# Kernel optimization log

Measured on AMD Instinct MI355X. Metric: run time of the kernel, lower is better.

## Reference

```python
import jax, jax.numpy as jnp
import numpy as np

STATE_LEN = 8
LAYER_NUM = 1
LN_EPS = 1e-5


def setup_inputs() -> dict:
    key = jax.random.key(0)
    ks = jax.random.split(key, 12)
    B, T, D = 4, 4096, 1024   # T = seq_len (4080) + 2*state_len (8)
    dk, dv = 128, 128
    s = 0.02
    f32 = jnp.float32
    return {
        "x": jax.random.normal(ks[0], (B, T, D), f32),
        # torch Linear(dim_input, 2*dim) without bias, stored as (in, out)
        "Wq": jax.random.normal(ks[1], (D, 2 * dk), f32) * s,
        "Wk": jax.random.normal(ks[2], (D, 2 * dk), f32) * s,
        "Wv": jax.random.normal(ks[3], (D, 2 * dv), f32) * s,
        "Wq_state": jax.random.normal(ks[4], (D, 2 * dk), f32) * s,
        "Wk_state": jax.random.normal(ks[5], (D, 2 * dk), f32) * s,
        "Wv_state": jax.random.normal(ks[6], (D, 2 * dv), f32) * s,
        "lambda_q1": jax.random.normal(ks[7], (1, dk), f32),
        "lambda_q2": jax.random.normal(ks[8], (1, dk), f32),
        "lambda_k1": jax.random.normal(ks[9], (dk, 1), f32),
        "lambda_k2": jax.random.normal(ks[10], (dk, 1), f32),
        "ln_gamma": jnp.ones((2 * dv,), f32),
        "ln_beta": jnp.zeros((2 * dv,), f32),
    }


def reference(x, Wq, Wk, Wv, Wq_state, Wk_state, Wv_state,
              lambda_q1, lambda_q2, lambda_k1, lambda_k2, ln_gamma, ln_beta):
    S = STATE_LEN
    lambda_init = 0.8 - 0.6 * np.exp(-0.3 * LAYER_NUM)  # python float, fp32-safe

    # extract_state: start state / middle / end state
    xs0, xm, xs1 = x[:, :S], x[:, S:-S], x[:, -S:]

    def proj(W, Ws):  # state tokens use *_state projections
        return jnp.concatenate([xs0 @ Ws, xm @ W, xs1 @ Ws], axis=1)

    q = proj(Wq, Wq_state)   # [B, T, 2*dk]
    k = proj(Wk, Wk_state)
    v = proj(Wv, Wv_state)   # [B, T, 2*dv]

    dk = Wq.shape[1] // 2
    q1, q2 = q[..., :dk], q[..., dk:]
    k1, k2 = k[..., :dk], k[..., dk:]

    T = q.shape[1]
    scale = 1.0 / jnp.sqrt(jnp.asarray(dk, q.dtype))  # SDPA default: 1/sqrt(dim_key)
    causal = jnp.tril(jnp.ones((T, T), dtype=bool))   # triu(-inf, diag=1) mask

    def attn(qh, kh):
        scores = jnp.einsum('btd,bsd->bts', qh, kh) * scale
        scores = jnp.where(causal, scores, -jnp.inf)
        p = jax.nn.softmax(scores, axis=-1)
        return jnp.einsum('bts,bse->bte', p, v)  # full 2*dv value

    att1 = attn(q1, k1)
    att2 = attn(q2, k2)

    lam = (jnp.exp(lambda_q1 @ lambda_k1) - jnp.exp(lambda_q2 @ lambda_k2))[0, 0] + lambda_init
    att = att1 - lam * att2  # [B, T, 2*dv]

    # out_norm: LayerNorm(2*dim_value, eps=1e-5)
    mu = jnp.mean(att, axis=-1, keepdims=True)
    var = jnp.var(att, axis=-1, keepdims=True)
    return (att - mu) / jnp.sqrt(var + LN_EPS) * ln_gamma + ln_beta
```

## Files before the change

### kernel.cpp

```cpp
#include <hip/hip_runtime.h>
#include <hip/hip_bf16.h>


typedef __bf16 bf16_t;
typedef __bf16 bf16x8 __attribute__((ext_vector_type(8)));
typedef __bf16 bf16x4 __attribute__((ext_vector_type(4)));
typedef float  f32x4  __attribute__((ext_vector_type(4)));

#define MFMA16(a, b, c) __builtin_amdgcn_mfma_f32_16x16x32_bf16((a), (b), (c), 0, 0, 0)

typedef __attribute__((address_space(1))) void glb_void;
typedef __attribute__((address_space(3))) void lds_void;

__device__ __forceinline__ void gld_lds16(void* dst, const void* src) {
  __builtin_amdgcn_global_load_lds((glb_void*)src, (lds_void*)dst, 16, 0, 0);
}

#define TSEQ 4096
#define C1f 0.12751744416f
#define C2f 4.3280851227f
#define LAM_INIT 0.3555090675909693f

__global__ void cvt_x_kernel(const float* __restrict__ x, bf16_t* __restrict__ xb) {
  size_t i = ((size_t)blockIdx.x * 256 + threadIdx.x) * 8;
  float4 a = *(const float4*)(x + i);
  float4 b = *(const float4*)(x + i + 4);
  bf16x8 o;
  o[0] = (bf16_t)a.x; o[1] = (bf16_t)a.y; o[2] = (bf16_t)a.z; o[3] = (bf16_t)a.w;
  o[4] = (bf16_t)b.x; o[5] = (bf16_t)b.y; o[6] = (bf16_t)b.z; o[7] = (bf16_t)b.w;
  *(bf16x8*)(xb + i) = o;
}

__global__ void cvt_w_kernel(const float* __restrict__ w0, const float* __restrict__ w1,
                             const float* __restrict__ w2, const float* __restrict__ w3,
                             const float* __restrict__ w4, const float* __restrict__ w5,
                             bf16_t* __restrict__ wt) {
  __shared__ float lt[64][68];
  const int mat = blockIdx.y;
  const int kt = blockIdx.x & 15, nt = blockIdx.x >> 4;
  const float* W = w0;
  if (mat == 1) W = w1; else if (mat == 2) W = w2; else if (mat == 3) W = w3;
  else if (mat == 4) W = w4; else if (mat == 5) W = w5;
  const int k0 = kt * 64, n0 = nt * 64;
  const int tid = threadIdx.x;
#pragma unroll
  for (int rnd = 0; rnd < 4; ++rnd) {
    int row = rnd * 16 + (tid >> 4);
    int c4 = (tid & 15) * 4;
    float4 v = *(const float4*)(W + (size_t)(k0 + row) * 256 + n0 + c4);
    *(float4*)&lt[row][c4] = v;
  }
  __syncthreads();
  const int n = tid >> 2;
  const int c16 = (tid & 3) * 16;
  bf16x8 o1, o2;
#pragma unroll
  for (int j = 0; j < 8; ++j) o1[j] = (bf16_t)lt[c16 + j][n];
#pragma unroll
  for (int j = 0; j < 8; ++j) o2[j] = (bf16_t)lt[c16 + 8 + j][n];
  bf16_t* dst = wt + (size_t)mat * 262144 + (size_t)(n0 + n) * 1024 + k0 + c16;
  *(bf16x8*)dst = o1;
  *(bf16x8*)(dst + 8) = o2;
}

__global__ void lam_kernel(const float* __restrict__ lq1, const float* __restrict__ lq2,
                           const float* __restrict__ lk1, const float* __restrict__ lk2,
                           float* __restrict__ lamout) {
  const int t = threadIdx.x;
  float s1 = lq1[2 * t] * lk1[2 * t] + lq1[2 * t + 1] * lk1[2 * t + 1];
  float s2 = lq2[2 * t] * lk2[2 * t] + lq2[2 * t + 1] * lk2[2 * t + 1];
#pragma unroll
  for (int m = 1; m < 64; m <<= 1) { s1 += __shfl_xor(s1, m); s2 += __shfl_xor(s2, m); }
  if (t == 0) *lamout = expf(s1) - expf(s2) + LAM_INIT;
}

__global__ __launch_bounds__(256, 2)
void proj_kernel(const bf16_t* __restrict__ xb, const bf16_t* __restrict__ wt,
                 bf16_t* __restrict__ qg, bf16_t* __restrict__ kg, bf16_t* __restrict__ vtg) {
  __shared__ __align__(16) char smem[49152];
  const int tid = threadIdx.x;
  const int w = tid >> 6;
  const int lane = tid & 63;
  const int l15 = lane & 15;
  const int g = lane >> 4;
  const int Mt = blockIdx.x;
  const int mat = blockIdx.y;
  const bf16_t* wmat = wt + (size_t)mat * 262144;
  const int row0 = Mt * 128;

  const f32x4 FZ = {0.f, 0.f, 0.f, 0.f};
  f32x4 acc[4][8];
#pragma unroll
  for (int i = 0; i < 4; ++i)
#pragma unroll
    for (int j = 0; j < 8; ++j) acc[i][j] = FZ;

  char* As = smem;
  char* Bs = smem + 16384;
  const int swz = (l15 & 7) << 4;

  for (int kt = 0; kt < 16; ++kt) {
    const int k0 = kt * 64;
#pragma unroll
    for (int rnd = 0; rnd < 4; ++rnd) {
      int arow = rnd * 32 + w * 8 + (lane >> 3);
      int m8 = lane & 7;
      const bf16_t* src = xb + (size_t)(row0 + arow) * 1024 + k0 + ((m8 ^ (arow & 7)) << 3);
      gld_lds16(As + rnd * 4096 + w * 1024, src);
    }
#pragma unroll
    for (int rnd = 0; rnd < 8; ++rnd) {
      int brow = rnd * 32 + w * 8 + (lane >> 3);
      int m8 = lane & 7;
      const bf16_t* src = wmat + (size_t)brow * 1024 + k0 + ((m8 ^ (brow & 7)) << 3);
      gld_lds16(Bs + rnd * 4096 + w * 1024, src);
    }
    __syncthreads();
    const int ab = (w >> 1) * 64;
    const int bb = (w & 1) * 128;
#pragma unroll
    for (int ks = 0; ks < 2; ++ks) {
      bf16x8 af[4], bfr[8];
#pragma unroll
      for (int mf = 0; mf < 4; ++mf) {
        int r = ab + mf * 16 + l15;
        af[mf] = *(const bf16x8*)(As + r * 128 + ((ks * 64 + g * 16) ^ swz));
      }
#pragma unroll
      for (int nf = 0; nf < 8; ++nf) {
        int c = bb + nf * 16 + l15;
        bfr[nf] = *(const bf16x8*)(Bs + c * 128 + ((ks * 64 + g * 16) ^ swz));
      }
#pragma unroll
      for (int mf = 0; mf < 4; ++mf)
#pragma unroll
        for (int nf = 0; nf < 8; ++nf)
          acc[mf][nf] = MFMA16(af[mf], bfr[nf], acc[mf][nf]);
    }
    __syncthreads();
  }

  const int ab = (w >> 1) * 64;
  const int bb = (w & 1) * 128;
  if (mat < 2) {
    bf16_t* og = (mat == 0) ? qg : kg;
#pragma unroll
    for (int mf = 0; mf < 4; ++mf)
#pragma unroll
      for (int nf = 0; nf < 8; ++nf) {
        int col = bb + nf * 16 + l15;
#pragma unroll
        for (int r = 0; r < 4; ++r) {
          int row = row0 + ab + mf * 16 + g * 4 + r;
          og[(size_t)row * 256 + col] = (bf16_t)acc[mf][nf][r];
        }
      }
  } else {
#pragma unroll
    for (int mf = 0; mf < 4; ++mf) {
      int t0 = row0 + ab + mf * 16 + g * 4;
      int bidx = t0 >> 12;
      int tt = t0 & 4095;
#pragma unroll
      for (int nf = 0; nf < 8; ++nf) {
        int col = bb + nf * 16 + l15;
        bf16x4 pk;
#pragma unroll
        for (int r = 0; r < 4; ++r) pk[r] = (bf16_t)acc[mf][nf][r];
        *(bf16x4*)(vtg + ((size_t)(bidx * 256 + col)) * 4096 + tt) = pk;
      }
    }
  }
}

__global__ void fixup_kernel(const bf16_t* __restrict__ xb, const bf16_t* __restrict__ wt,
                             bf16_t* __restrict__ qg, bf16_t* __restrict__ kg,
                             bf16_t* __restrict__ vtg) {
  __shared__ bf16_t xs[1024];
  const int bx = blockIdx.x, mat = blockIdx.y;
  const int b = bx >> 4, j = bx & 15;
  const int t = (j < 8) ? j : (4080 + j);
  const size_t row = (size_t)b * 4096 + t;
  const int tid = threadIdx.x;
  *(bf16x4*)&xs[tid * 4] = *(const bf16x4*)(xb + row * 1024 + tid * 4);
  __syncthreads();
  const bf16_t* wrow = wt + (size_t)(mat + 3) * 262144 + (size_t)tid * 1024;
  float acc = 0.f;
#pragma unroll 4
  for (int kk = 0; kk < 128; ++kk) {
    bf16x8 w8 = *(const bf16x8*)(wrow + kk * 8);
    bf16x8 x8 = *(const bf16x8*)(&xs[kk * 8]);
#pragma unroll
    for (int q = 0; q < 8; ++q) acc += (float)x8[q] * (float)w8[q];
  }
  if (mat == 0)      qg[row * 256 + tid] = (bf16_t)acc;
  else if (mat == 1) kg[row * 256 + tid] = (bf16_t)acc;
  else               vtg[((size_t)(b * 256 + tid)) * 4096 + t] = (bf16_t)acc;
}

#define SM_KB 0
#define SM_VB 65536
#define SM_P  131072
#define SM_G  153600
#define SM_B  154624
#define SM_TOT 155648

__global__ __launch_bounds__(256, 1)
void attn_kernel(const bf16_t* __restrict__ qg, const bf16_t* __restrict__ kg,
                 const bf16_t* __restrict__ vtg, const float* __restrict__ lamp,
                 const float* __restrict__ gamma, const float* __restrict__ beta,
                 float* __restrict__ out) {
  __shared__ __align__(16) char smem[SM_TOT];
  const int tid = threadIdx.x;
  const int w = tid >> 6;
  const int lane = tid & 63;
  const int l15 = lane & 15;
  const int g = lane >> 4;
  const int tile = (int)blockIdx.x >> 2;
  const int b = (int)blockIdx.x & 3;

  *(float*)(smem + SM_G + tid * 4) = gamma[tid];
  *(float*)(smem + SM_B + tid * 4) = beta[tid];

  const bf16_t* qb = qg + ((size_t)(b * 4096 + tile * 64 + w * 16 + l15)) * 256;
  bf16x8 q1f[4], q2f[4];
#pragma unroll
  for (int ks = 0; ks < 4; ++ks) {
    q1f[ks] = *(const bf16x8*)(qb + ks * 32 + g * 8);
    q2f[ks] = *(const bf16x8*)(qb + 128 + ks * 32 + g * 8);
  }

  const f32x4 FZ = {0.f, 0.f, 0.f, 0.f};
  f32x4 acc1[16], acc2[16];
#pragma unroll
  for (int i = 0; i < 16; ++i) { acc1[i] = FZ; acc2[i] = FZ; }
  float l1a[4] = {0.f, 0.f, 0.f, 0.f}, l2a[4] = {0.f, 0.f, 0.f, 0.f};

  const int nkb = tile + 1;
  char* P1 = smem + SM_P + w * 5632;
  char* P2 = P1 + 2816;
  const int swz = (l15 & 7) << 4;

#define STAGE_KV(KB, BUF) do {                                                          \
    const int kr_ = (KB) * 64;                                                          \
    char* kdst_ = smem + SM_KB + (BUF) * 32768;                                         \
    char* vdst_ = smem + SM_VB + (BUF) * 32768;                                         \
    _Pragma("unroll")                                                                   \
    for (int rnd = 0; rnd < 8; ++rnd) {                                                 \
      int row_ = rnd * 8 + w * 2 + (lane >> 5);                                         \
      int mm_ = lane & 31;                                                              \
      const bf16_t* src_ = kg + (((size_t)(b * 4096 + kr_ + row_)) << 8)                \
                              + ((mm_ ^ (row_ & 7)) << 3);                              \
      gld_lds16(kdst_ + rnd * 4096 + w * 1024, src_);                                   \
    }                                                                                   \
    _Pragma("unroll")                                                                   \
    for (int rnd = 0; rnd < 8; ++rnd) {                                                 \
      int ch_ = rnd * 32 + w * 8 + (lane >> 3);                                         \
      int m8_ = lane & 7;                                                               \
      const bf16_t* src_ = vtg + ((size_t)(b * 256 + ch_)) * 4096 + kr_                 \
                               + ((m8_ ^ (ch_ & 7)) << 3);                              \
      gld_lds16(vdst_ + rnd * 4096 + w * 1024, src_);                                   \
    }                                                                                   \
  } while (0)

  STAGE_KV(0, 0);
  __syncthreads();

  for (int kb = 0; kb < nkb; ++kb) {
    const int cur = kb & 1;
    if (kb + 1 < nkb) STAGE_KV(kb + 1, cur ^ 1);

    const char* kbp = smem + SM_KB + cur * 32768;
    const char* vbp = smem + SM_VB + cur * 32768;

    f32x4 S1[4], S2[4];
#pragma unroll
    for (int nf = 0; nf < 4; ++nf) {
      f32x4 a1 = {0.f, 0.f, 0.f, 0.f}, a2 = {0.f, 0.f, 0.f, 0.f};
      const int krow = nf * 16 + l15;
#pragma unroll
      for (int ks = 0; ks < 4; ++ks) {
        bf16x8 kf1 = *(const bf16x8*)(kbp + krow * 512 + ((ks * 64 + g * 16) ^ swz));
        a1 = MFMA16(q1f[ks], kf1, a1);
        bf16x8 kf2 = *(const bf16x8*)(kbp + krow * 512 + ((256 + ks * 64 + g * 16) ^ swz));
        a2 = MFMA16(q2f[ks], kf2, a2);
      }
      S1[nf] = a1; S2[nf] = a2;
    }

    const bool lastkb = (kb == tile);
#pragma unroll
    for (int nf = 0; nf < 4; ++nf) {
#pragma unroll
      for (int r = 0; r < 4; ++r) {
        float p1 = exp2f(fmaf(S1[nf][r], C1f, -C2f));
        float p2 = exp2f(fmaf(S2[nf][r], C1f, -C2f));
        if (lastkb) {
          const int kl = nf * 16 + l15;
          const int ql = w * 16 + g * 4 + r;
          if (kl > ql) { p1 = 0.f; p2 = 0.f; }
        }
        bf16_t pb1 = (bf16_t)p1, pb2 = (bf16_t)p2;
        l1a[r] += (float)pb1;
        l2a[r] += (float)pb2;
        *(bf16_t*)(P1 + (g * 4 + r) * 176 + (nf * 16 + l15) * 2) = pb1;
        *(bf16_t*)(P2 + (g * 4 + r) * 176 + (nf * 16 + l15) * 2) = pb2;
      }
    }

#pragma unroll
    for (int ks = 0; ks < 2; ++ks) {
      bf16x8 p1a = *(const bf16x8*)(P1 + l15 * 176 + ks * 64 + g * 16);
      bf16x8 p2a = *(const bf16x8*)(P2 + l15 * 176 + ks * 64 + g * 16);
#pragma unroll
      for (int nf = 0; nf < 16; ++nf) {
        const int ch = nf * 16 + l15;
        bf16x8 vf = *(const bf16x8*)(vbp + ch * 128 + ((ks * 64 + g * 16) ^ swz));
        acc1[nf] = MFMA16(p1a, vf, acc1[nf]);
        acc2[nf] = MFMA16(p2a, vf, acc2[nf]);
      }
    }
    __syncthreads();
  }

  const float lam = lamp[0];
  const float* gs = (const float*)(smem + SM_G);
  const float* bs = (const float*)(smem + SM_B);
  float l1r[4], l2r[4];
#pragma unroll
  for (int r = 0; r < 4; ++r) {
    float a = l1a[r], c = l2a[r];
#pragma unroll
    for (int m = 1; m < 16; m <<= 1) { a += __shfl_xor(a, m); c += __shfl_xor(c, m); }
    l1r[r] = 1.f / a; l2r[r] = 1.f / c;
  }
#pragma unroll
  for (int nf = 0; nf < 16; ++nf)
#pragma unroll
    for (int r = 0; r < 4; ++r)
      acc1[nf][r] = acc1[nf][r] * l1r[r] - lam * acc2[nf][r] * l2r[r];

#pragma unroll
  for (int r = 0; r < 4; ++r) {
    float s = 0.f, s2 = 0.f;
#pragma unroll
    for (int nf = 0; nf < 16; ++nf) { float v = acc1[nf][r]; s += v; s2 += v * v; }
#pragma unroll
    for (int m = 1; m < 16; m <<= 1) { s += __shfl_xor(s, m); s2 += __shfl_xor(s2, m); }
    const float mu = s * (1.f / 256.f);
    const float var = s2 * (1.f / 256.f) - mu * mu;
    const float rstd = rsqrtf(var + 1e-5f);
    const int qrow = tile * 64 + w * 16 + g * 4 + r;
    float* orow = out + ((size_t)(b * 4096 + qrow)) * 256;
#pragma unroll
    for (int nf = 0; nf < 16; ++nf) {
      const int ch = nf * 16 + l15;
      orow[ch] = (acc1[nf][r] - mu) * rstd * gs[ch] + bs[ch];
    }
  }
}

extern "C" void kernel_launch(void* const* d_in, const int* in_sizes, int n_in,
                              void* d_out, int out_size, void* d_ws, size_t ws_size,
                              hipStream_t stream) {
  (void)in_sizes; (void)n_in; (void)out_size; (void)ws_size;
  const float* x   = (const float*)d_in[0];
  const float* Wq  = (const float*)d_in[1];
  const float* Wk  = (const float*)d_in[2];
  const float* Wv  = (const float*)d_in[3];
  const float* Wqs = (const float*)d_in[4];
  const float* Wks = (const float*)d_in[5];
  const float* Wvs = (const float*)d_in[6];
  const float* lq1 = (const float*)d_in[7];
  const float* lq2 = (const float*)d_in[8];
  const float* lk1 = (const float*)d_in[9];
  const float* lk2 = (const float*)d_in[10];
  const float* gam = (const float*)d_in[11];
  const float* bet = (const float*)d_in[12];
  float* out = (float*)d_out;

  char* ws = (char*)d_ws;
  float* lam   = (float*)ws;
  bf16_t* xb   = (bf16_t*)(ws + 256);
  bf16_t* wt   = (bf16_t*)(ws + 256 + 33554432);
  bf16_t* qgb  = (bf16_t*)(ws + 256 + 33554432 + 3145728);
  bf16_t* kgb  = qgb + 4194304;
  bf16_t* vtgb = kgb + 4194304;

  cvt_x_kernel<<<8192, 256, 0, stream>>>(x, xb);
  cvt_w_kernel<<<dim3(64, 6), 256, 0, stream>>>(Wq, Wk, Wv, Wqs, Wks, Wvs, wt);
  lam_kernel<<<1, 64, 0, stream>>>(lq1, lq2, lk1, lk2, lam);
  proj_kernel<<<dim3(128, 3), 256, 0, stream>>>(xb, wt, qgb, kgb, vtgb);
  fixup_kernel<<<dim3(64, 3), 256, 0, stream>>>(xb, wt, qgb, kgb, vtgb);
  attn_kernel<<<256, 256, 0, stream>>>(qgb, kgb, vtgb, lam, gam, bet, out);
}
```

Before: 394.0 us.

## Rewrite attention kernel with 512 threads splitting heads and channel slices

Replaces the attention kernel with one that uses 8 waves per block. The waves split the two softmax heads and four value-channel slices, and key blocks shrink to 32 keys. K and V staging moves from direct global-to-LDS loads to register-staged loads written into padded LDS rows, and LDS use drops to about 88KB so two blocks can share a CU. The head difference and LayerNorm reductions now cross waves through LDS, which adds barriers and doubles the number of loop iterations.

```diff
diff --git a/kernel.cpp b/kernel.cpp
--- a/kernel.cpp
+++ b/kernel.cpp
@@ -16,7 +16,6 @@
   __builtin_amdgcn_global_load_lds((glb_void*)src, (lds_void*)dst, 16, 0, 0);
 }
 
-#define TSEQ 4096
 #define C1f 0.12751744416f
 #define C2f 4.3280851227f
 #define LAM_INIT 0.3555090675909693f
@@ -198,165 +197,216 @@
   else               vtg[((size_t)(b * 256 + tid)) * 4096 + t] = (bf16_t)acc;
 }
 
-#define SM_KB 0
-#define SM_VB 65536
-#define SM_P  131072
-#define SM_G  153600
-#define SM_B  154624
-#define SM_TOT 155648
-
-__global__ __launch_bounds__(256, 1)
-void attn_kernel(const bf16_t* __restrict__ qg, const bf16_t* __restrict__ kg,
-                 const bf16_t* __restrict__ vtg, const float* __restrict__ lamp,
-                 const float* __restrict__ gamma, const float* __restrict__ beta,
-                 float* __restrict__ out) {
-  __shared__ __align__(16) char smem[SM_TOT];
+#define LDS_K 0
+#define LDS_V 33792
+#define LDS_P 74752
+#define LDS_L 84992
+#define LDS_S 86016
+#define LDS_TOT 88064
+#define KROW 528
+#define VROW 80
+#define PROW 80
+
+__global__ __launch_bounds__(512, 2)
+void attn2_kernel(const bf16_t* __restrict__ qg, const bf16_t* __restrict__ kg,
+                  const bf16_t* __restrict__ vtg, const float* __restrict__ lamp,
+                  const float* __restrict__ gamma, const float* __restrict__ beta,
+                  float* __restrict__ out) {
+  __shared__ __align__(16) char smem[LDS_TOT];
   const int tid = threadIdx.x;
-  const int w = tid >> 6;
-  const int lane = tid & 63;
-  const int l15 = lane & 15;
-  const int g = lane >> 4;
-  const int tile = (int)blockIdx.x >> 2;
-  const int b = (int)blockIdx.x & 3;
-
-  *(float*)(smem + SM_G + tid * 4) = gamma[tid];
-  *(float*)(smem + SM_B + tid * 4) = beta[tid];
-
-  const bf16_t* qb = qg + ((size_t)(b * 4096 + tile * 64 + w * 16 + l15)) * 256;
-  bf16x8 q1f[4], q2f[4];
-#pragma unroll
-  for (int ks = 0; ks < 4; ++ks) {
-    q1f[ks] = *(const bf16x8*)(qb + ks * 32 + g * 8);
-    q2f[ks] = *(const bf16x8*)(qb + 128 + ks * 32 + g * 8);
-  }
+  const int w = tid >> 6, lane = tid & 63;
+  const int l15 = lane & 15, g = lane >> 4;
+  const int h = w & 1, sl = (w >> 1) & 1, half = w >> 2;
+  const int cslice = half * 2 + sl;
+  const int t = (int)blockIdx.x >> 2, b = (int)blockIdx.x & 3;
+  const int ns = 2 * t + 2;
+  const size_t qrow0 = (size_t)b * 4096 + (size_t)t * 64;
+
+  bf16x8 Qf[2][4];
+#pragma unroll
+  for (int qfl = 0; qfl < 2; ++qfl)
+#pragma unroll
+    for (int ks = 0; ks < 4; ++ks)
+      Qf[qfl][ks] = *(const bf16x8*)(qg + (qrow0 + (half * 2 + qfl) * 16 + l15) * 256
+                                        + h * 128 + ks * 32 + g * 8);
 
   const f32x4 FZ = {0.f, 0.f, 0.f, 0.f};
-  f32x4 acc1[16], acc2[16];
-#pragma unroll
-  for (int i = 0; i < 16; ++i) { acc1[i] = FZ; acc2[i] = FZ; }
-  float l1a[4] = {0.f, 0.f, 0.f, 0.f}, l2a[4] = {0.f, 0.f, 0.f, 0.f};
-
-  const int nkb = tile + 1;
-  char* P1 = smem + SM_P + w * 5632;
-  char* P2 = P1 + 2816;
-  const int swz = (l15 & 7) << 4;
-
-#define STAGE_KV(KB, BUF) do {                                                          \
-    const int kr_ = (KB) * 64;                                                          \
-    char* kdst_ = smem + SM_KB + (BUF) * 32768;                                         \
-    char* vdst_ = smem + SM_VB + (BUF) * 32768;                                         \
-    _Pragma("unroll")                                                                   \
-    for (int rnd = 0; rnd < 8; ++rnd) {                                                 \
-      int row_ = rnd * 8 + w * 2 + (lane >> 5);                                         \
-      int mm_ = lane & 31;                                                              \
-      const bf16_t* src_ = kg + (((size_t)(b * 4096 + kr_ + row_)) << 8)                \
-                              + ((mm_ ^ (row_ & 7)) << 3);                              \
-      gld_lds16(kdst_ + rnd * 4096 + w * 1024, src_);                                   \
-    }                                                                                   \
-    _Pragma("unroll")                                                                   \
-    for (int rnd = 0; rnd < 8; ++rnd) {                                                 \
-      int ch_ = rnd * 32 + w * 8 + (lane >> 3);                                         \
-      int m8_ = lane & 7;                                                               \
-      const bf16_t* src_ = vtg + ((size_t)(b * 256 + ch_)) * 4096 + kr_                 \
-                               + ((m8_ ^ (ch_ & 7)) << 3);                              \
-      gld_lds16(vdst_ + rnd * 4096 + w * 1024, src_);                                   \
-    }                                                                                   \
+  f32x4 acc[4][4];
+#pragma unroll
+  for (int i = 0; i < 4; ++i)
+#pragma unroll
+    for (int j = 0; j < 4; ++j) acc[i][j] = FZ;
+  float lpart[2][4] = {{0.f,0.f,0.f,0.f},{0.f,0.f,0.f,0.f}};
+
+  int4 kstg[2], vstg[2];
+  const bf16_t* kB = kg + ((size_t)b << 12) * 256;
+  const bf16_t* vB = vtg + ((size_t)b * 256) * 4096;
+
+#define STAGE_LOAD(STEP) do { const int key0_ = 32 * (STEP);                              \
+    kstg[0] = *(const int4*)(kB + (size_t)(key0_ + w * 4 + (lane >> 5)) * 256 + (lane & 31) * 8);     \
+    kstg[1] = *(const int4*)(kB + (size_t)(key0_ + w * 4 + 2 + (lane >> 5)) * 256 + (lane & 31) * 8); \
+    vstg[0] = *(const int4*)(vB + (size_t)(w * 32 + (lane >> 2)) * 4096 + key0_ + (lane & 3) * 8);    \
+    vstg[1] = *(const int4*)(vB + (size_t)(w * 32 + 16 + (lane >> 2)) * 4096 + key0_ + (lane & 3) * 8); \
   } while (0)
-
-  STAGE_KV(0, 0);
-  __syncthreads();
-
-  for (int kb = 0; kb < nkb; ++kb) {
-    const int cur = kb & 1;
-    if (kb + 1 < nkb) STAGE_KV(kb + 1, cur ^ 1);
-
-    const char* kbp = smem + SM_KB + cur * 32768;
-    const char* vbp = smem + SM_VB + cur * 32768;
-
-    f32x4 S1[4], S2[4];
-#pragma unroll
-    for (int nf = 0; nf < 4; ++nf) {
-      f32x4 a1 = {0.f, 0.f, 0.f, 0.f}, a2 = {0.f, 0.f, 0.f, 0.f};
-      const int krow = nf * 16 + l15;
-#pragma unroll
-      for (int ks = 0; ks < 4; ++ks) {
-        bf16x8 kf1 = *(const bf16x8*)(kbp + krow * 512 + ((ks * 64 + g * 16) ^ swz));
-        a1 = MFMA16(q1f[ks], kf1, a1);
-        bf16x8 kf2 = *(const bf16x8*)(kbp + krow * 512 + ((256 + ks * 64 + g * 16) ^ swz));
-        a2 = MFMA16(q2f[ks], kf2, a2);
-      }
-      S1[nf] = a1; S2[nf] = a2;
-    }
-
-    const bool lastkb = (kb == tile);
-#pragma unroll
-    for (int nf = 0; nf < 4; ++nf) {
+#define STAGE_WRITE(BUF) do {                                                             \
+    *(int4*)(smem + LDS_K + (BUF) * 16896 + (w * 4 + (lane >> 5)) * KROW + (lane & 31) * 16) = kstg[0];     \
+    *(int4*)(smem + LDS_K + (BUF) * 16896 + (w * 4 + 2 + (lane >> 5)) * KROW + (lane & 31) * 16) = kstg[1]; \
+    *(int4*)(smem + LDS_V + (BUF) * 20480 + (w * 32 + (lane >> 2)) * VROW + (lane & 3) * 16) = vstg[0];     \
+    *(int4*)(smem + LDS_V + (BUF) * 20480 + (w * 32 + 16 + (lane >> 2)) * VROW + (lane & 3) * 16) = vstg[1];\
+  } while (0)
+
+  STAGE_LOAD(0); STAGE_WRITE(0);
+  __syncthreads();
+
+  int cur = 0;
+  for (int s = 0; s < ns; ++s) {
+    const bool more = (s + 1 < ns);
+    if (more) STAGE_LOAD(s + 1);
+
+    const char* kb = smem + LDS_K + cur * 16896;
+    f32x4 S[2] = {FZ, FZ};
+#pragma unroll
+    for (int ks = 0; ks < 4; ++ks) {
+      bf16x8 kf = *(const bf16x8*)(kb + (sl * 16 + l15) * KROW + h * 256 + ks * 64 + g * 16);
+      S[0] = MFMA16(Qf[0][ks], kf, S[0]);
+      S[1] = MFMA16(Qf[1][ks], kf, S[1]);
+    }
+
+    const int keyg = 32 * s + sl * 16 + l15;
+    const int qg0 = 64 * t;
+#pragma unroll
+    for (int qfl = 0; qfl < 2; ++qfl) {
+      const int qf = half * 2 + qfl;
 #pragma unroll
       for (int r = 0; r < 4; ++r) {
-        float p1 = exp2f(fmaf(S1[nf][r], C1f, -C2f));
-        float p2 = exp2f(fmaf(S2[nf][r], C1f, -C2f));
-        if (lastkb) {
-          const int kl = nf * 16 + l15;
-          const int ql = w * 16 + g * 4 + r;
-          if (kl > ql) { p1 = 0.f; p2 = 0.f; }
+        float p = exp2f(fmaf(S[qfl][r], C1f, -C2f));
+        const int qloc = qf * 16 + g * 4 + r;
+        if (keyg > qg0 + qloc) p = 0.f;
+        bf16_t pb = (bf16_t)p;
+        lpart[qfl][r] += (float)pb;
+        *(bf16_t*)(smem + LDS_P + h * 5120 + qloc * PROW + (sl * 16 + l15) * 2) = pb;
+      }
+    }
+    __syncthreads();
+
+    const char* vb = smem + LDS_V + cur * 20480;
+    bf16x8 Pf[4], Vf[4];
+#pragma unroll
+    for (int qf = 0; qf < 4; ++qf)
+      Pf[qf] = *(const bf16x8*)(smem + LDS_P + h * 5120 + (qf * 16 + l15) * PROW + g * 16);
+#pragma unroll
+    for (int chf = 0; chf < 4; ++chf)
+      Vf[chf] = *(const bf16x8*)(vb + (cslice * 64 + chf * 16 + l15) * VROW + g * 16);
+#pragma unroll
+    for (int qf = 0; qf < 4; ++qf)
+#pragma unroll
+      for (int chf = 0; chf < 4; ++chf)
+        acc[qf][chf] = MFMA16(Pf[qf], Vf[chf], acc[qf][chf]);
+
+    if (more) STAGE_WRITE(cur ^ 1);
+    __syncthreads();
+    cur ^= 1;
+  }
+
+#pragma unroll
+  for (int qfl = 0; qfl < 2; ++qfl)
+#pragma unroll
+    for (int r = 0; r < 4; ++r) {
+      float v = lpart[qfl][r];
+#pragma unroll
+      for (int m = 1; m < 16; m <<= 1) v += __shfl_xor(v, m);
+      if (l15 == 0)
+        *(float*)(smem + LDS_L + (((h * 2 + sl) * 64) + (half * 2 + qfl) * 16 + g * 4 + r) * 4) = v;
+    }
+  __syncthreads();
+
+  const float lam = lamp[0];
+  float rl[4][4];
+#pragma unroll
+  for (int qf = 0; qf < 4; ++qf)
+#pragma unroll
+    for (int r = 0; r < 4; ++r) {
+      const int q = qf * 16 + g * 4 + r;
+      float lsum = *(const float*)(smem + LDS_L + ((h * 2) * 64 + q) * 4)
+                 + *(const float*)(smem + LDS_L + ((h * 2 + 1) * 64 + q) * 4);
+      rl[qf][r] = 1.f / lsum;
+    }
+
+  if (h == 1) {
+#pragma unroll
+    for (int qf = 0; qf < 4; ++qf)
+#pragma unroll
+      for (int chf = 0; chf < 4; ++chf) {
+        f32x4 e;
+#pragma unroll
+        for (int r = 0; r < 4; ++r) e[r] = lam * acc[qf][chf][r] * rl[qf][r];
+        *(f32x4*)(smem + (cslice * 64 + chf * 16 + l15) * 256 + (qf * 16 + g * 4) * 4) = e;
+      }
+  }
+  __syncthreads();
+
+  if (h == 0) {
+    float s1v[4][4], s2v[4][4];
+#pragma unroll
+    for (int qf = 0; qf < 4; ++qf)
+#pragma unroll
+      for (int r = 0; r < 4; ++r) { s1v[qf][r] = 0.f; s2v[qf][r] = 0.f; }
+#pragma unroll
+    for (int qf = 0; qf < 4; ++qf)
+#pragma unroll
+      for (int chf = 0; chf < 4; ++chf) {
+        f32x4 e = *(const f32x4*)(smem + (cslice * 64 + chf * 16 + l15) * 256 + (qf * 16 + g * 4) * 4);
+#pragma unroll
+        for (int r = 0; r < 4; ++r) {
+          float dv = acc[qf][chf][r] * rl[qf][r] - e[r];
+          acc[qf][chf][r] = dv;
+          s1v[qf][r] += dv;
+          s2v[qf][r] += dv * dv;
         }
-        bf16_t pb1 = (bf16_t)p1, pb2 = (bf16_t)p2;
-        l1a[r] += (float)pb1;
-        l2a[r] += (float)pb2;
-        *(bf16_t*)(P1 + (g * 4 + r) * 176 + (nf * 16 + l15) * 2) = pb1;
-        *(bf16_t*)(P2 + (g * 4 + r) * 176 + (nf * 16 + l15) * 2) = pb2;
-      }
-    }
-
-#pragma unroll
-    for (int ks = 0; ks < 2; ++ks) {
-      bf16x8 p1a = *(const bf16x8*)(P1 + l15 * 176 + ks * 64 + g * 16);
-      bf16x8 p2a = *(const bf16x8*)(P2 + l15 * 176 + ks * 64 + g * 16);
-#pragma unroll
-      for (int nf = 0; nf < 16; ++nf) {
-        const int ch = nf * 16 + l15;
-        bf16x8 vf = *(const bf16x8*)(vbp + ch * 128 + ((ks * 64 + g * 16) ^ swz));
-        acc1[nf] = MFMA16(p1a, vf, acc1[nf]);
-        acc2[nf] = MFMA16(p2a, vf, acc2[nf]);
-      }
-    }
-    __syncthreads();
-  }
-
-  const float lam = lamp[0];
-  const float* gs = (const float*)(smem + SM_G);
-  const float* bs = (const float*)(smem + SM_B);
-  float l1r[4], l2r[4];
-#pragma unroll
-  for (int r = 0; r < 4; ++r) {
-    float a = l1a[r], c = l2a[r];
-#pragma unroll
-    for (int m = 1; m < 16; m <<= 1) { a += __shfl_xor(a, m); c += __shfl_xor(c, m); }
-    l1r[r] = 1.f / a; l2r[r] = 1.f / c;
-  }
-#pragma unroll
-  for (int nf = 0; nf < 16; ++nf)
-#pragma unroll
-    for (int r = 0; r < 4; ++r)
-      acc1[nf][r] = acc1[nf][r] * l1r[r] - lam * acc2[nf][r] * l2r[r];
-
-#pragma unroll
-  for (int r = 0; r < 4; ++r) {
-    float s = 0.f, s2 = 0.f;
-#pragma unroll
-    for (int nf = 0; nf < 16; ++nf) { float v = acc1[nf][r]; s += v; s2 += v * v; }
-#pragma unroll
-    for (int m = 1; m < 16; m <<= 1) { s += __shfl_xor(s, m); s2 += __shfl_xor(s2, m); }
-    const float mu = s * (1.f / 256.f);
-    const float var = s2 * (1.f / 256.f) - mu * mu;
-    const float rstd = rsqrtf(var + 1e-5f);
-    const int qrow = tile * 64 + w * 16 + g * 4 + r;
-    float* orow = out + ((size_t)(b * 4096 + qrow)) * 256;
-#pragma unroll
-    for (int nf = 0; nf < 16; ++nf) {
-      const int ch = nf * 16 + l15;
-      orow[ch] = (acc1[nf][r] - mu) * rstd * gs[ch] + bs[ch];
-    }
+      }
+#pragma unroll
+    for (int qf = 0; qf < 4; ++qf)
+#pragma unroll
+      for (int r = 0; r < 4; ++r) {
+        float a = s1v[qf][r], c = s2v[qf][r];
+#pragma unroll
+        for (int m = 1; m < 16; m <<= 1) { a += __shfl_xor(a, m); c += __shfl_xor(c, m); }
+        if (l15 == 0) {
+          const int q = qf * 16 + g * 4 + r;
+          *(float*)(smem + LDS_S + (cslice * 64 + q) * 4) = a;
+          *(float*)(smem + LDS_S + ((4 + cslice) * 64 + q) * 4) = c;
+        }
+      }
+  }
+  __syncthreads();
+
+  if (h == 0) {
+    float gm[4], bt[4];
+#pragma unroll
+    for (int chf = 0; chf < 4; ++chf) {
+      const int ch = cslice * 64 + chf * 16 + l15;
+      gm[chf] = gamma[ch];
+      bt[chf] = beta[ch];
+    }
+#pragma unroll
+    for (int qf = 0; qf < 4; ++qf)
+#pragma unroll
+      for (int r = 0; r < 4; ++r) {
+        const int q = qf * 16 + g * 4 + r;
+        float ssum = 0.f, s2um = 0.f;
+#pragma unroll
+        for (int cs = 0; cs < 4; ++cs) {
+          ssum += *(const float*)(smem + LDS_S + (cs * 64 + q) * 4);
+          s2um += *(const float*)(smem + LDS_S + ((4 + cs) * 64 + q) * 4);
+        }
+        const float mu = ssum * (1.f / 256.f);
+        const float var = s2um * (1.f / 256.f) - mu * mu;
+        const float rstd = rsqrtf(var + 1e-5f);
+        float* orow = out + (qrow0 + q) * 256;
+#pragma unroll
+        for (int chf = 0; chf < 4; ++chf)
+          orow[cslice * 64 + chf * 16 + l15] = (acc[qf][chf][r] - mu) * rstd * gm[chf] + bt[chf];
+      }
   }
 }
 
@@ -392,5 +442,5 @@
   lam_kernel<<<1, 64, 0, stream>>>(lq1, lq2, lk1, lk2, lam);
   proj_kernel<<<dim3(128, 3), 256, 0, stream>>>(xb, wt, qgb, kgb, vtgb);
   fixup_kernel<<<dim3(64, 3), 256, 0, stream>>>(xb, wt, qgb, kgb, vtgb);
-  attn_kernel<<<256, 256, 0, stream>>>(qgb, kgb, vtgb, lam, gam, bet, out);
-}
+  attn2_kernel<<<256, 512, 0, stream>>>(qgb, kgb, vtgb, lam, gam, bet, out);
+}
```

Measured after the change: 413.1 us. 1.05x slower.
